# Kernel optimization log

Measured on AMD Instinct MI355X. Metric: run time of the kernel, lower is better.

Reference implementation:

```python
import jax, jax.numpy as jnp
import numpy as np

# e2m1 FP4 value table: sign bit in nibble MSB, values {0,0.5,1,1.5,2,3,4,6}
_E2M1 = jnp.array([0.0, 0.5, 1.0, 1.5, 2.0, 3.0, 4.0, 6.0,
                   -0.0, -0.5, -1.0, -1.5, -2.0, -3.0, -4.0, -6.0], dtype=jnp.float32)


def _dequant_fp4(packed, scales, group_size):
    """packed: [E, out, in//8] uint32; scales: [E, in//group_size, out] -> [E, out, in] f32."""
    shifts = jnp.arange(8, dtype=jnp.uint32) * 4  # nibble shift amounts 0,4,...,28
    nib = (packed[..., None] >> shifts) & jnp.uint32(0xF)  # [E, out, in//8, 8]
    E, O, P, _ = nib.shape
    nib = nib.reshape(E, O, P * 8).astype(jnp.int32)
    w = _E2M1[nib]  # [E, out, in] f32
    gids = jnp.arange(P * 8) // group_size  # group id per input column
    sc = jnp.transpose(scales, (0, 2, 1))[:, :, gids]  # [E, out, in]
    return w * sc


def setup_inputs() -> dict:
    E, H, I, T, K, G = 8, 2048, 1408, 2048, 2, 128
    key = jax.random.key(0)
    ks = jax.random.split(key, 9)
    x = jax.random.normal(ks[0], (T, H), dtype=jnp.float32)
    gate_packed = jax.random.bits(ks[1], (E, I, H // 8), dtype=jnp.uint32)
    up_packed = jax.random.bits(ks[2], (E, I, H // 8), dtype=jnp.uint32)
    down_packed = jax.random.bits(ks[3], (E, H, I // 8), dtype=jnp.uint32)
    gate_scales = jax.random.uniform(ks[4], (E, H // G, I), jnp.float32, 0.5, 1.5)
    up_scales = jax.random.uniform(ks[5], (E, H // G, I), jnp.float32, 0.5, 1.5)
    down_scales = jax.random.uniform(ks[6], (E, I // G, H), jnp.float32, 0.5, 1.5)
    topk_idx = jax.random.randint(ks[7], (T, K), 0, E, dtype=jnp.int32)
    w = jax.random.uniform(ks[8], (T, K), jnp.float32)
    topk_w = w / jnp.sum(w, axis=-1, keepdims=True)
    return {"x": x,
            "gate_packed": gate_packed, "gate_scales": gate_scales,
            "up_packed": up_packed, "up_scales": up_scales,
            "down_packed": down_packed, "down_scales": down_scales,
            "topk_idx": topk_idx, "topk_w": topk_w, "group_size": G}


def reference(x, gate_packed, gate_scales, up_packed, up_scales,
              down_packed, down_scales, topk_idx, topk_w, group_size):
    # Fused dequant (nibble unpack + e2m1 table + per-group scale) for all experts
    gate_w = _dequant_fp4(gate_packed, gate_scales, group_size)  # [E, I, H]
    up_w = _dequant_fp4(up_packed, up_scales, group_size)        # [E, I, H]
    down_w = _dequant_fp4(down_packed, down_scales, group_size)  # [E, H, I]
    # Grouped SwiGLU expert MLP (dense over E=8 experts, gather routed outputs)
    g = jnp.einsum('th,eih->eti', x, gate_w)
    u = jnp.einsum('th,eih->eti', x, up_w)
    h = jax.nn.silu(g) * u                                        # [E, T, I]
    y = jnp.einsum('eti,ehi->eth', h, down_w)                     # [E, T, H]
    T = x.shape[0]
    sel = y[topk_idx, jnp.arange(T)[:, None], :]                  # [T, K, H]
    return jnp.sum(sel * topk_w[..., None], axis=1)               # [T, H]
```

## Files before the change

kernel.cpp:

```cpp
#include <hip/hip_runtime.h>
#include <hip/hip_bf16.h>
#include <stdint.h>

#define E_ 8
#define H_ 2048
#define I_ 1408
#define T_ 2048
#define K_ 2
#define G_ 128

typedef __bf16 bf16;
typedef bf16 bf16x8 __attribute__((ext_vector_type(8)));
typedef float f32x4 __attribute__((ext_vector_type(4)));

__device__ __forceinline__ uint32_t prm(uint32_t hi, uint32_t lo, uint32_t sel) {
    return __builtin_amdgcn_perm(hi, lo, sel);
}

struct DequantTab { uint32_t thi0, thi1, tlo0, tlo1; };

__device__ __forceinline__ DequantTab build_tab(float s) {
    union { bf16 h[8]; uint32_t u[4]; } tb;
    tb.h[0] = (bf16)(0.0f);
    tb.h[1] = (bf16)(0.5f * s);
    tb.h[2] = (bf16)(1.0f * s);
    tb.h[3] = (bf16)(1.5f * s);
    tb.h[4] = (bf16)(2.0f * s);
    tb.h[5] = (bf16)(3.0f * s);
    tb.h[6] = (bf16)(4.0f * s);
    tb.h[7] = (bf16)(6.0f * s);
    DequantTab t;
    t.thi0 = prm(tb.u[1], tb.u[0], 0x07050301u);
    t.tlo0 = prm(tb.u[1], tb.u[0], 0x06040200u);
    t.thi1 = prm(tb.u[3], tb.u[2], 0x07050301u);
    t.tlo1 = prm(tb.u[3], tb.u[2], 0x06040200u);
    return t;
}

__device__ __forceinline__ uint4 dequant8t(uint32_t p, const DequantTab& t) {
    const uint32_t pr = p >> 4;
    const uint32_t pe = p  & 0x07070707u;
    const uint32_t po = pr & 0x07070707u;
    const uint32_t He = prm(t.thi1, t.thi0, pe) | ((p  & 0x08080808u) << 4);
    const uint32_t Le = prm(t.tlo1, t.tlo0, pe);
    const uint32_t Ho = prm(t.thi1, t.thi0, po) | ((pr & 0x08080808u) << 4);
    const uint32_t Lo = prm(t.tlo1, t.tlo0, po);
    const uint32_t E01 = prm(He, Le, 0x05010400u);
    const uint32_t E23 = prm(He, Le, 0x07030602u);
    const uint32_t O01 = prm(Ho, Lo, 0x05010400u);
    const uint32_t O23 = prm(Ho, Lo, 0x07030602u);
    return make_uint4(prm(O01, E01, 0x05040100u),
                      prm(O01, E01, 0x07060302u),
                      prm(O23, E23, 0x05040100u),
                      prm(O23, E23, 0x07060302u));
}

__device__ __forceinline__ void gld16(void* lds, const void* g) {
    __builtin_amdgcn_global_load_lds(
        (__attribute__((address_space(1))) void*)g,
        (__attribute__((address_space(3))) void*)lds, 16, 0, 0);
}

__global__ void route_count(const int* __restrict__ topk_idx, int* __restrict__ counts) {
    int p = blockIdx.x * blockDim.x + threadIdx.x;
    if (p < T_ * K_) atomicAdd(&counts[topk_idx[p]], 1);
}

__global__ void route_scan(const int* __restrict__ counts, int* __restrict__ offsets,
                           int* __restrict__ tmap) {
    if (threadIdx.x == 0) {
        int acc = 0, ti = 0;
        for (int e = 0; e < E_; e++) {
            offsets[e] = acc;
            int nt = (counts[e] + 127) >> 7;
            for (int j = 0; j < nt; j++) tmap[ti++] = (e << 16) | j;
            acc += counts[e];
        }
        offsets[E_] = acc;
        for (; ti < 64; ti++) tmap[ti] = -1;
    }
}

__global__ void route_fill(const int* __restrict__ topk_idx, const float* __restrict__ topk_w,
                           int* __restrict__ cursors, const int* __restrict__ offsets,
                           int* __restrict__ tok, float* __restrict__ wgt,
                           int* __restrict__ inv) {
    int p = blockIdx.x * blockDim.x + threadIdx.x;
    if (p < T_ * K_) {
        int e = topk_idx[p];
        int slot = atomicAdd(&cursors[e], 1);
        int idx = offsets[e] + slot;
        tok[idx] = p / K_;
        wgt[idx] = topk_w[p];
        inv[p] = idx;
    }
}

__global__ __launch_bounds__(256)
void xcast_kernel(const float* __restrict__ x, uint4* __restrict__ xb) {
    const int i = blockIdx.x * 256 + threadIdx.x;
    const float4 a = ((const float4*)x)[i * 2];
    const float4 b = ((const float4*)x)[i * 2 + 1];
    union { uint4 u; bf16 h[8]; } r;
    r.h[0] = (bf16)a.x; r.h[1] = (bf16)a.y; r.h[2] = (bf16)a.z; r.h[3] = (bf16)a.w;
    r.h[4] = (bf16)b.x; r.h[5] = (bf16)b.y; r.h[6] = (bf16)b.z; r.h[7] = (bf16)b.w;
    xb[i] = r.u;
}

__global__ __launch_bounds__(256, 3)
void gemm1q_kernel(const bf16* __restrict__ xb,
                   const uint32_t* __restrict__ gate_packed,
                   const float* __restrict__ gate_scales,
                   const uint32_t* __restrict__ up_packed,
                   const float* __restrict__ up_scales,
                   const int* __restrict__ offsets,
                   const int* __restrict__ tmap,
                   const int* __restrict__ tok, bf16* __restrict__ h_buf)
{
    const int tm = tmap[blockIdx.x];
    if (tm < 0) return;
    const int e = tm >> 16, ty = tm & 0xffff;
    const int row0 = offsets[e];
    const int cnt = offsets[e + 1] - row0;
    const int itile = blockIdx.y;

    __shared__ __align__(16) bf16 xs[2][128][64];
    __shared__ __align__(16) bf16 wgs[64][64];
    __shared__ __align__(16) bf16 wus[64][64];
    __shared__ int toks[128];

    const int tid = threadIdx.x;
    if (tid < 128) {
        int r = ty * 128 + tid;
        toks[tid] = tok[row0 + ((r < cnt) ? r : (cnt - 1))];
    }
    __syncthreads();

    const bf16* xsrc[4];
    int xf[4];
#pragma unroll
    for (int i = 0; i < 4; i++) {
        const int f = i * 256 + tid;
        const int r = f >> 3, c = f & 7;
        xf[i] = f;
        xsrc[i] = xb + (size_t)toks[r] * H_ + ((c ^ (r & 7)) * 8);
    }

    const int mat  = tid >> 7;
    const int id   = tid & 127;
    const int wrow = id >> 1;
    const int quad = id & 1;
    const int irow = itile * 64 + wrow;
    const uint32_t* wp = (mat ? up_packed : gate_packed)
        + (size_t)e * I_ * (H_ / 8) + (size_t)irow * (H_ / 8) + quad * 4;
    const float* ws_row = (mat ? up_scales : gate_scales)
        + (size_t)e * (H_ / G_) * I_ + irow;
    bf16 (* const wdst)[64] = mat ? wus : wgs;
    const int cb = quad * 4, rs = wrow & 7;

    const int wave = tid >> 6, lane = tid & 63;
    const int wy = wave >> 1, wx = wave & 1;
    const int lrow = lane & 15, kq = lane >> 4;

    f32x4 accg[4][2] = {};
    f32x4 accu[4][2] = {};

    uint4 pw = *(const uint4*)wp;
    DequantTab tw = build_tab(ws_row[0]);
#pragma unroll
    for (int i = 0; i < 4; i++)
        gld16((char*)&xs[0][0][0] + xf[i] * 16, xsrc[i]);
    {
        uint4 d0 = dequant8t(pw.x, tw), d1 = dequant8t(pw.y, tw);
        uint4 d2 = dequant8t(pw.z, tw), d3 = dequant8t(pw.w, tw);
        *(uint4*)&wdst[wrow][((cb + 0) ^ rs) * 8] = d0;
        *(uint4*)&wdst[wrow][((cb + 1) ^ rs) * 8] = d1;
        *(uint4*)&wdst[wrow][((cb + 2) ^ rs) * 8] = d2;
        *(uint4*)&wdst[wrow][((cb + 3) ^ rs) * 8] = d3;
    }
    __syncthreads();

    for (int ks = 0; ks < 32; ks++) {
        const int b = ks & 1;
        const bool hasn = (ks < 31);
        uint4 pw_n;
        if (hasn) {
            pw_n = *(const uint4*)(wp + (ks + 1) * 8);
#pragma unroll
            for (int i = 0; i < 4; i++)
                gld16((char*)&xs[b ^ 1][0][0] + xf[i] * 16, xsrc[i] + (ks + 1) * 64);
        }
#pragma unroll
        for (int kh = 0; kh < 2; kh++) {
            bf16x8 a[4], bg[2], bu[2];
#pragma unroll
            for (int mi = 0; mi < 4; mi++) {
                const int ra = wy * 64 + mi * 16 + lrow;
                a[mi] = *(const bf16x8*)&xs[b][ra][((kh * 4 + kq) ^ (ra & 7)) * 8];
            }
#pragma unroll
            for (int ni = 0; ni < 2; ni++) {
                const int rb = wx * 32 + ni * 16 + lrow;
                const int cc = ((kh * 4 + kq) ^ (rb & 7)) * 8;
                bg[ni] = *(const bf16x8*)&wgs[rb][cc];
                bu[ni] = *(const bf16x8*)&wus[rb][cc];
            }
#pragma unroll
            for (int mi = 0; mi < 4; mi++)
#pragma unroll
                for (int ni = 0; ni < 2; ni++) {
                    accg[mi][ni] = __builtin_amdgcn_mfma_f32_16x16x32_bf16(a[mi], bg[ni], accg[mi][ni], 0, 0, 0);
                    accu[mi][ni] = __builtin_amdgcn_mfma_f32_16x16x32_bf16(a[mi], bu[ni], accu[mi][ni], 0, 0, 0);
                }
        }
        __syncthreads();
        if (hasn) {
            if (ks & 1) tw = build_tab(ws_row[((ks + 1) >> 1) * I_]);
            uint4 d0 = dequant8t(pw_n.x, tw), d1 = dequant8t(pw_n.y, tw);
            uint4 d2 = dequant8t(pw_n.z, tw), d3 = dequant8t(pw_n.w, tw);
            *(uint4*)&wdst[wrow][((cb + 0) ^ rs) * 8] = d0;
            *(uint4*)&wdst[wrow][((cb + 1) ^ rs) * 8] = d1;
            *(uint4*)&wdst[wrow][((cb + 2) ^ rs) * 8] = d2;
            *(uint4*)&wdst[wrow][((cb + 3) ^ rs) * 8] = d3;
            __syncthreads();
        }
    }

#pragma unroll
    for (int mi = 0; mi < 4; mi++)
#pragma unroll
        for (int ni = 0; ni < 2; ni++) {
            const int icol = itile * 64 + wx * 32 + ni * 16 + lrow;
#pragma unroll
            for (int r = 0; r < 4; r++) {
                const int grow = ty * 128 + wy * 64 + mi * 16 + kq * 4 + r;
                if (grow < cnt) {
                    const float gv = accg[mi][ni][r];
                    const float hv = gv / (1.f + __expf(-gv)) * accu[mi][ni][r];
                    h_buf[(size_t)(row0 + grow) * I_ + icol] = (bf16)hv;
                }
            }
        }
}

__global__ __launch_bounds__(256, 3)
void gemm2q_kernel(const bf16* __restrict__ h_buf,
                   const uint32_t* __restrict__ down_packed,
                   const float* __restrict__ down_scales,
                   const int* __restrict__ offsets,
                   const int* __restrict__ tmap,
                   const float* __restrict__ wgt, float* __restrict__ yp)
{
    const int tm = tmap[blockIdx.x];
    if (tm < 0) return;
    const int e = tm >> 16, ty = tm & 0xffff;
    const int row0 = offsets[e];
    const int cnt = offsets[e + 1] - row0;
    const int htile = blockIdx.y;

    __shared__ __align__(16) bf16 hs[2][128][64];
    __shared__ __align__(16) bf16 wds[128][64];

    const int tid = threadIdx.x;

    const bf16* hsrc[4];
    int hf[4];
#pragma unroll
    for (int i = 0; i < 4; i++) {
        const int f = i * 256 + tid;
        const int r = f >> 3, c = f & 7;
        int g = ty * 128 + r;  g = (g < cnt) ? g : (cnt - 1);
        hf[i] = f;
        hsrc[i] = h_buf + (size_t)(row0 + g) * I_ + ((c ^ (r & 7)) * 8);
    }

    const int wrow = tid >> 1;
    const int quad = tid & 1;
    const int hrow = htile * 128 + wrow;
    const uint32_t* dp = down_packed + (size_t)e * H_ * (I_ / 8) + (size_t)hrow * (I_ / 8) + quad * 4;
    const float* ds_row = down_scales + (size_t)e * (I_ / G_) * H_ + hrow;
    const int cb = quad * 4, rs = wrow & 7;

    const int wave = tid >> 6, lane = tid & 63;
    const int wy = wave >> 1, wx = wave & 1;
    const int lrow = lane & 15, kq = lane >> 4;

    f32x4 acc[4][4] = {};

    uint4 pw = *(const uint4*)dp;
    DequantTab tw = build_tab(ds_row[0]);
#pragma unroll
    for (int i = 0; i < 4; i++)
        gld16((char*)&hs[0][0][0] + hf[i] * 16, hsrc[i]);
    {
        uint4 d0 = dequant8t(pw.x, tw), d1 = dequant8t(pw.y, tw);
        uint4 d2 = dequant8t(pw.z, tw), d3 = dequant8t(pw.w, tw);
        *(uint4*)&wds[wrow][((cb + 0) ^ rs) * 8] = d0;
        *(uint4*)&wds[wrow][((cb + 1) ^ rs) * 8] = d1;
        *(uint4*)&wds[wrow][((cb + 2) ^ rs) * 8] = d2;
        *(uint4*)&wds[wrow][((cb + 3) ^ rs) * 8] = d3;
    }
    __syncthreads();

    for (int ks = 0; ks < I_ / 64; ks++) {
        const int b = ks & 1;
        const bool hasn = (ks < I_ / 64 - 1);
        uint4 pw_n;
        if (hasn) {
            pw_n = *(const uint4*)(dp + (ks + 1) * 8);
#pragma unroll
            for (int i = 0; i < 4; i++)
                gld16((char*)&hs[b ^ 1][0][0] + hf[i] * 16, hsrc[i] + (ks + 1) * 64);
        }
#pragma unroll
        for (int kh = 0; kh < 2; kh++) {
            bf16x8 a[4], bb[4];
#pragma unroll
            for (int mi = 0; mi < 4; mi++) {
                const int ra = wy * 64 + mi * 16 + lrow;
                a[mi] = *(const bf16x8*)&hs[b][ra][((kh * 4 + kq) ^ (ra & 7)) * 8];
            }
#pragma unroll
            for (int ni = 0; ni < 4; ni++) {
                const int rb = wx * 64 + ni * 16 + lrow;
                bb[ni] = *(const bf16x8*)&wds[rb][((kh * 4 + kq) ^ (rb & 7)) * 8];
            }
#pragma unroll
            for (int mi = 0; mi < 4; mi++)
#pragma unroll
                for (int ni = 0; ni < 4; ni++)
                    acc[mi][ni] = __builtin_amdgcn_mfma_f32_16x16x32_bf16(a[mi], bb[ni], acc[mi][ni], 0, 0, 0);
        }
        __syncthreads();
        if (hasn) {
            if (ks & 1) tw = build_tab(ds_row[((ks + 1) >> 1) * H_]);
            uint4 d0 = dequant8t(pw_n.x, tw), d1 = dequant8t(pw_n.y, tw);
            uint4 d2 = dequant8t(pw_n.z, tw), d3 = dequant8t(pw_n.w, tw);
            *(uint4*)&wds[wrow][((cb + 0) ^ rs) * 8] = d0;
            *(uint4*)&wds[wrow][((cb + 1) ^ rs) * 8] = d1;
            *(uint4*)&wds[wrow][((cb + 2) ^ rs) * 8] = d2;
            *(uint4*)&wds[wrow][((cb + 3) ^ rs) * 8] = d3;
            __syncthreads();
        }
    }

#pragma unroll
    for (int mi = 0; mi < 4; mi++)
#pragma unroll
        for (int r = 0; r < 4; r++) {
            const int grow = ty * 128 + wy * 64 + mi * 16 + kq * 4 + r;
            if (grow < cnt) {
                const float w = wgt[row0 + grow];
#pragma unroll
                for (int ni = 0; ni < 4; ni++) {
                    const int col = htile * 128 + wx * 64 + ni * 16 + lrow;
                    yp[(size_t)(row0 + grow) * H_ + col] = acc[mi][ni][r] * w;
                }
            }
        }
}

__global__ __launch_bounds__(256)
void combine_kernel(const float* __restrict__ yp, const int* __restrict__ inv,
                    float* __restrict__ out) {
    const int idx = blockIdx.x * 256 + threadIdx.x;
    const int t = idx >> 9;
    const int c = idx & 511;
    const float4 a = ((const float4*)yp)[(size_t)inv[t * 2] * (H_ / 4) + c];
    const float4 b = ((const float4*)yp)[(size_t)inv[t * 2 + 1] * (H_ / 4) + c];
    float4 o;
    o.x = a.x + b.x; o.y = a.y + b.y; o.z = a.z + b.z; o.w = a.w + b.w;
    ((float4*)out)[idx] = o;
}

extern "C" void kernel_launch(void* const* d_in, const int* in_sizes, int n_in,
                              void* d_out, int out_size, void* d_ws, size_t ws_size,
                              hipStream_t stream) {
    const float* x = (const float*)d_in[0];
    const uint32_t* gate_packed = (const uint32_t*)d_in[1];
    const float* gate_scales = (const float*)d_in[2];
    const uint32_t* up_packed = (const uint32_t*)d_in[3];
    const float* up_scales = (const float*)d_in[4];
    const uint32_t* down_packed = (const uint32_t*)d_in[5];
    const float* down_scales = (const float*)d_in[6];
    const int* topk_idx = (const int*)d_in[7];
    const float* topk_w = (const float*)d_in[8];
    float* out = (float*)d_out;

    char* ws = (char*)d_ws;
    int* counts  = (int*)ws;
    int* cursors = (int*)(ws + 32);
    int* offsets = (int*)(ws + 64);
    int* tmap    = (int*)(ws + 128);
    int* tok     = (int*)(ws + 640);
    float* wgt   = (float*)(ws + 17024);
    int* inv     = (int*)(ws + 33408);
    bf16* h_buf  = (bf16*)(ws + 49792);
    bf16* xb     = (bf16*)(ws + 49792 + 11534336ull);
    float* yp    = (float*)(ws + 49792 + 11534336ull + 8388608ull);

    hipMemsetAsync(d_ws, 0, 1024, stream);

    route_count<<<(T_ * K_ + 255) / 256, 256, 0, stream>>>(topk_idx, counts);
    route_scan<<<1, 64, 0, stream>>>(counts, offsets, tmap);
    route_fill<<<(T_ * K_ + 255) / 256, 256, 0, stream>>>(topk_idx, topk_w, cursors, offsets,
                                                          tok, wgt, inv);
    xcast_kernel<<<T_ * H_ / 8 / 256, 256, 0, stream>>>(x, (uint4*)xb);

    dim3 g1(40, I_ / 64);
    gemm1q_kernel<<<g1, 256, 0, stream>>>(xb, gate_packed, gate_scales, up_packed, up_scales,
                                          offsets, tmap, tok, h_buf);
    dim3 g2(40, H_ / 128);
    gemm2q_kernel<<<g2, 256, 0, stream>>>(h_buf, down_packed, down_scales,
                                          offsets, tmap, wgt, yp);
    combine_kernel<<<T_ * H_ / 4 / 256, 256, 0, stream>>>(yp, inv, out);
}
```

Before: 291.8 us.

## Double-buffer dequantized weight tiles to drop the second barrier per k-step

Both grouped GEMM kernels now keep two LDS buffers for the dequantized FP4 weights. The next weight tile is dequantized into the spare buffer before the MFMA loop of the current step, packed weights and scales are prefetched one step further ahead, and one of the two __syncthreads per iteration goes away. The aim is to overlap dequant ALU work with matrix math and cut barrier stalls. The cost is more LDS and registers, so launch bounds drop from 3 to 2 blocks per CU, which lowers occupancy.

```diff
diff --git a/kernel.cpp b/kernel.cpp
--- a/kernel.cpp
+++ b/kernel.cpp
@@ -107,8 +107,8 @@
     xb[i] = r.u;
 }
 
-__global__ __launch_bounds__(256, 3)
-void gemm1q_kernel(const bf16* __restrict__ xb,
+__global__ __launch_bounds__(256, 2)
+void gemm1d_kernel(const bf16* __restrict__ xb,
                    const uint32_t* __restrict__ gate_packed,
                    const float* __restrict__ gate_scales,
                    const uint32_t* __restrict__ up_packed,
@@ -125,8 +125,8 @@
     const int itile = blockIdx.y;
 
     __shared__ __align__(16) bf16 xs[2][128][64];
-    __shared__ __align__(16) bf16 wgs[64][64];
-    __shared__ __align__(16) bf16 wus[64][64];
+    __shared__ __align__(16) bf16 wgs[2][64][64];
+    __shared__ __align__(16) bf16 wus[2][64][64];
     __shared__ int toks[128];
 
     const int tid = threadIdx.x;
@@ -155,7 +155,6 @@
         + (size_t)e * I_ * (H_ / 8) + (size_t)irow * (H_ / 8) + quad * 4;
     const float* ws_row = (mat ? up_scales : gate_scales)
         + (size_t)e * (H_ / G_) * I_ + irow;
-    bf16 (* const wdst)[64] = mat ? wus : wgs;
     const int cb = quad * 4, rs = wrow & 7;
 
     const int wave = tid >> 6, lane = tid & 63;
@@ -165,30 +164,43 @@
     f32x4 accg[4][2] = {};
     f32x4 accu[4][2] = {};
 
-    uint4 pw = *(const uint4*)wp;
+    uint4 pw_cur = *(const uint4*)wp;
+    uint4 pw_nxt = *(const uint4*)(wp + 8);
     DequantTab tw = build_tab(ws_row[0]);
+    float s_pend = ws_row[I_];
 #pragma unroll
     for (int i = 0; i < 4; i++)
         gld16((char*)&xs[0][0][0] + xf[i] * 16, xsrc[i]);
     {
-        uint4 d0 = dequant8t(pw.x, tw), d1 = dequant8t(pw.y, tw);
-        uint4 d2 = dequant8t(pw.z, tw), d3 = dequant8t(pw.w, tw);
-        *(uint4*)&wdst[wrow][((cb + 0) ^ rs) * 8] = d0;
-        *(uint4*)&wdst[wrow][((cb + 1) ^ rs) * 8] = d1;
-        *(uint4*)&wdst[wrow][((cb + 2) ^ rs) * 8] = d2;
-        *(uint4*)&wdst[wrow][((cb + 3) ^ rs) * 8] = d3;
+        bf16 (* const wd)[64] = (mat ? wus : wgs)[0];
+        uint4 d0 = dequant8t(pw_cur.x, tw), d1 = dequant8t(pw_cur.y, tw);
+        uint4 d2 = dequant8t(pw_cur.z, tw), d3 = dequant8t(pw_cur.w, tw);
+        *(uint4*)&wd[wrow][((cb + 0) ^ rs) * 8] = d0;
+        *(uint4*)&wd[wrow][((cb + 1) ^ rs) * 8] = d1;
+        *(uint4*)&wd[wrow][((cb + 2) ^ rs) * 8] = d2;
+        *(uint4*)&wd[wrow][((cb + 3) ^ rs) * 8] = d3;
     }
     __syncthreads();
 
     for (int ks = 0; ks < 32; ks++) {
         const int b = ks & 1;
-        const bool hasn = (ks < 31);
-        uint4 pw_n;
-        if (hasn) {
-            pw_n = *(const uint4*)(wp + (ks + 1) * 8);
+        if (ks < 31) {
 #pragma unroll
             for (int i = 0; i < 4; i++)
                 gld16((char*)&xs[b ^ 1][0][0] + xf[i] * 16, xsrc[i] + (ks + 1) * 64);
+            if (ks & 1) {
+                tw = build_tab(s_pend);
+                int ng = (ks + 3) >> 1; if (ng > H_ / G_ - 1) ng = H_ / G_ - 1;
+                s_pend = ws_row[ng * I_];
+            }
+            bf16 (* const wd)[64] = (mat ? wus : wgs)[b ^ 1];
+            uint4 d0 = dequant8t(pw_nxt.x, tw), d1 = dequant8t(pw_nxt.y, tw);
+            uint4 d2 = dequant8t(pw_nxt.z, tw), d3 = dequant8t(pw_nxt.w, tw);
+            *(uint4*)&wd[wrow][((cb + 0) ^ rs) * 8] = d0;
+            *(uint4*)&wd[wrow][((cb + 1) ^ rs) * 8] = d1;
+            *(uint4*)&wd[wrow][((cb + 2) ^ rs) * 8] = d2;
+            *(uint4*)&wd[wrow][((cb + 3) ^ rs) * 8] = d3;
+            if (ks < 30) pw_nxt = *(const uint4*)(wp + (ks + 2) * 8);
         }
 #pragma unroll
         for (int kh = 0; kh < 2; kh++) {
@@ -202,8 +214,8 @@
             for (int ni = 0; ni < 2; ni++) {
                 const int rb = wx * 32 + ni * 16 + lrow;
                 const int cc = ((kh * 4 + kq) ^ (rb & 7)) * 8;
-                bg[ni] = *(const bf16x8*)&wgs[rb][cc];
-                bu[ni] = *(const bf16x8*)&wus[rb][cc];
+                bg[ni] = *(const bf16x8*)&wgs[b][rb][cc];
+                bu[ni] = *(const bf16x8*)&wus[b][rb][cc];
             }
 #pragma unroll
             for (int mi = 0; mi < 4; mi++)
@@ -214,16 +226,6 @@
                 }
         }
         __syncthreads();
-        if (hasn) {
-            if (ks & 1) tw = build_tab(ws_row[((ks + 1) >> 1) * I_]);
-            uint4 d0 = dequant8t(pw_n.x, tw), d1 = dequant8t(pw_n.y, tw);
-            uint4 d2 = dequant8t(pw_n.z, tw), d3 = dequant8t(pw_n.w, tw);
-            *(uint4*)&wdst[wrow][((cb + 0) ^ rs) * 8] = d0;
-            *(uint4*)&wdst[wrow][((cb + 1) ^ rs) * 8] = d1;
-            *(uint4*)&wdst[wrow][((cb + 2) ^ rs) * 8] = d2;
-            *(uint4*)&wdst[wrow][((cb + 3) ^ rs) * 8] = d3;
-            __syncthreads();
-        }
     }
 
 #pragma unroll
@@ -243,8 +245,8 @@
         }
 }
 
-__global__ __launch_bounds__(256, 3)
-void gemm2q_kernel(const bf16* __restrict__ h_buf,
+__global__ __launch_bounds__(256, 2)
+void gemm2d_kernel(const bf16* __restrict__ h_buf,
                    const uint32_t* __restrict__ down_packed,
                    const float* __restrict__ down_scales,
                    const int* __restrict__ offsets,
@@ -259,7 +261,7 @@
     const int htile = blockIdx.y;
 
     __shared__ __align__(16) bf16 hs[2][128][64];
-    __shared__ __align__(16) bf16 wds[128][64];
+    __shared__ __align__(16) bf16 wds[2][128][64];
 
     const int tid = threadIdx.x;
 
@@ -287,30 +289,42 @@
 
     f32x4 acc[4][4] = {};
 
-    uint4 pw = *(const uint4*)dp;
+    uint4 pw_cur = *(const uint4*)dp;
+    uint4 pw_nxt = *(const uint4*)(dp + 8);
     DequantTab tw = build_tab(ds_row[0]);
+    float s_pend = ds_row[H_];
 #pragma unroll
     for (int i = 0; i < 4; i++)
         gld16((char*)&hs[0][0][0] + hf[i] * 16, hsrc[i]);
     {
-        uint4 d0 = dequant8t(pw.x, tw), d1 = dequant8t(pw.y, tw);
-        uint4 d2 = dequant8t(pw.z, tw), d3 = dequant8t(pw.w, tw);
-        *(uint4*)&wds[wrow][((cb + 0) ^ rs) * 8] = d0;
-        *(uint4*)&wds[wrow][((cb + 1) ^ rs) * 8] = d1;
-        *(uint4*)&wds[wrow][((cb + 2) ^ rs) * 8] = d2;
-        *(uint4*)&wds[wrow][((cb + 3) ^ rs) * 8] = d3;
+        uint4 d0 = dequant8t(pw_cur.x, tw), d1 = dequant8t(pw_cur.y, tw);
+        uint4 d2 = dequant8t(pw_cur.z, tw), d3 = dequant8t(pw_cur.w, tw);
+        *(uint4*)&wds[0][wrow][((cb + 0) ^ rs) * 8] = d0;
+        *(uint4*)&wds[0][wrow][((cb + 1) ^ rs) * 8] = d1;
+        *(uint4*)&wds[0][wrow][((cb + 2) ^ rs) * 8] = d2;
+        *(uint4*)&wds[0][wrow][((cb + 3) ^ rs) * 8] = d3;
     }
     __syncthreads();
 
-    for (int ks = 0; ks < I_ / 64; ks++) {
+    const int NS = I_ / 64;
+    for (int ks = 0; ks < NS; ks++) {
         const int b = ks & 1;
-        const bool hasn = (ks < I_ / 64 - 1);
-        uint4 pw_n;
-        if (hasn) {
-            pw_n = *(const uint4*)(dp + (ks + 1) * 8);
+        if (ks < NS - 1) {
 #pragma unroll
             for (int i = 0; i < 4; i++)
                 gld16((char*)&hs[b ^ 1][0][0] + hf[i] * 16, hsrc[i] + (ks + 1) * 64);
+            if (ks & 1) {
+                tw = build_tab(s_pend);
+                int ng = (ks + 3) >> 1; if (ng > I_ / G_ - 1) ng = I_ / G_ - 1;
+                s_pend = ds_row[ng * H_];
+            }
+            uint4 d0 = dequant8t(pw_nxt.x, tw), d1 = dequant8t(pw_nxt.y, tw);
+            uint4 d2 = dequant8t(pw_nxt.z, tw), d3 = dequant8t(pw_nxt.w, tw);
+            *(uint4*)&wds[b ^ 1][wrow][((cb + 0) ^ rs) * 8] = d0;
+            *(uint4*)&wds[b ^ 1][wrow][((cb + 1) ^ rs) * 8] = d1;
+            *(uint4*)&wds[b ^ 1][wrow][((cb + 2) ^ rs) * 8] = d2;
+            *(uint4*)&wds[b ^ 1][wrow][((cb + 3) ^ rs) * 8] = d3;
+            if (ks < NS - 2) pw_nxt = *(const uint4*)(dp + (ks + 2) * 8);
         }
 #pragma unroll
         for (int kh = 0; kh < 2; kh++) {
@@ -323,7 +337,7 @@
 #pragma unroll
             for (int ni = 0; ni < 4; ni++) {
                 const int rb = wx * 64 + ni * 16 + lrow;
-                bb[ni] = *(const bf16x8*)&wds[rb][((kh * 4 + kq) ^ (rb & 7)) * 8];
+                bb[ni] = *(const bf16x8*)&wds[b][rb][((kh * 4 + kq) ^ (rb & 7)) * 8];
             }
 #pragma unroll
             for (int mi = 0; mi < 4; mi++)
@@ -332,16 +346,6 @@
                     acc[mi][ni] = __builtin_amdgcn_mfma_f32_16x16x32_bf16(a[mi], bb[ni], acc[mi][ni], 0, 0, 0);
         }
         __syncthreads();
-        if (hasn) {
-            if (ks & 1) tw = build_tab(ds_row[((ks + 1) >> 1) * H_]);
-            uint4 d0 = dequant8t(pw_n.x, tw), d1 = dequant8t(pw_n.y, tw);
-            uint4 d2 = dequant8t(pw_n.z, tw), d3 = dequant8t(pw_n.w, tw);
-            *(uint4*)&wds[wrow][((cb + 0) ^ rs) * 8] = d0;
-            *(uint4*)&wds[wrow][((cb + 1) ^ rs) * 8] = d1;
-            *(uint4*)&wds[wrow][((cb + 2) ^ rs) * 8] = d2;
-            *(uint4*)&wds[wrow][((cb + 3) ^ rs) * 8] = d3;
-            __syncthreads();
-        }
     }
 
 #pragma unroll
@@ -408,10 +412,10 @@
     xcast_kernel<<<T_ * H_ / 8 / 256, 256, 0, stream>>>(x, (uint4*)xb);
 
     dim3 g1(40, I_ / 64);
-    gemm1q_kernel<<<g1, 256, 0, stream>>>(xb, gate_packed, gate_scales, up_packed, up_scales,
+    gemm1d_kernel<<<g1, 256, 0, stream>>>(xb, gate_packed, gate_scales, up_packed, up_scales,
                                           offsets, tmap, tok, h_buf);
     dim3 g2(40, H_ / 128);
-    gemm2q_kernel<<<g2, 256, 0, stream>>>(h_buf, down_packed, down_scales,
+    gemm2d_kernel<<<g2, 256, 0, stream>>>(h_buf, down_packed, down_scales,
                                           offsets, tmap, wgt, yp);
     combine_kernel<<<T_ * H_ / 4 / 256, 256, 0, stream>>>(yp, inv, out);
 }
```

Measured after the change: 291.9 us. Within noise of the previous version (+0.0%).
